# Kernel optimization log

Hardware: AMD Instinct MI355X
Metric: run time of the kernel (lower is better)

The kernel has to match this reference:

```python
import jax, jax.numpy as jnp
import numpy as np

NUM_NEIGHBORS = 1000

def setup_inputs() -> dict:
    key = jax.random.key(0)
    k1, k2, k3 = jax.random.split(key, 3)
    N, R, H, O = 1024, 100000, 512, 256
    x = jax.random.normal(k1, (N, H), dtype=jnp.float32)
    ref_x = jax.random.normal(k2, (R, H), dtype=jnp.float32)
    ref_y = jax.random.normal(k3, (R, O), dtype=jnp.float32)
    return {"x": x, "ref_x": ref_x, "ref_y": ref_y}

def reference(x, ref_x, ref_y):
    # encoder1 modeled as identity (x is the encoded embedding)
    xn = x / jnp.linalg.norm(x, axis=-1, keepdims=True)          # [N, H]
    rn = ref_x / jnp.linalg.norm(ref_x, axis=-1, keepdims=True)  # [R, H]
    sim = jnp.einsum('nh,rh->nr', xn, rn)                        # [N, R] cosine sims
    knn_vals, knn_idx = jax.lax.top_k(sim, NUM_NEIGHBORS)        # [N, K]
    weight = jax.nn.softmax(knn_vals, axis=1)                    # [N, K]
    neigh_y = ref_y[knn_idx]                                     # [N, K, O]
    pred_y = jnp.einsum('nko,nk->no', neigh_y, weight)           # [N, O]
    return pred_y
```

## Files before the change

kernel.cpp:

```cpp
#include <hip/hip_runtime.h>
#include <hip/hip_bf16.h>
#include <hip/hip_fp16.h>
#include <stdint.h>

#define NQ 1024
#define NR 100000
#define NH 512
#define NO 256
#define NK 1000
#define NBINS 4096
#define DEF_CAP 1024
#define CND_CAP 768
#define DELTA 2.0e-3f

typedef __attribute__((ext_vector_type(8))) short bf16x8;
typedef __attribute__((ext_vector_type(4))) float f32x4;
typedef __attribute__((address_space(3))) void lds_void;
typedef const __attribute__((address_space(1))) void glb_void;

static __device__ inline uint32_t pack_bf16_trunc(float lo, float hi) {
    return __builtin_amdgcn_perm(__float_as_uint(hi), __float_as_uint(lo), 0x07060302u);
}

__global__ __launch_bounds__(256) void conv_norm_kernel(const float* __restrict__ src,
                                                        int rows,
                                                        ushort* __restrict__ dst_bf,
                                                        double* __restrict__ inv_out)
{
    const int wave = threadIdx.x >> 6;
    const int lane = threadIdx.x & 63;
    const int row  = blockIdx.x * 4 + wave;
    if (row >= rows) return;
    const float* p = src + (size_t)row * NH + lane * 8;
    float4 v0 = *(const float4*)p;
    float4 v1 = *(const float4*)(p + 4);
    double s = (double)v0.x * v0.x + (double)v0.y * v0.y
             + (double)v0.z * v0.z + (double)v0.w * v0.w
             + (double)v1.x * v1.x + (double)v1.y * v1.y
             + (double)v1.z * v1.z + (double)v1.w * v1.w;
    uint4 pk;
    pk.x = pack_bf16_trunc(v0.x, v0.y);
    pk.y = pack_bf16_trunc(v0.z, v0.w);
    pk.z = pack_bf16_trunc(v1.x, v1.y);
    pk.w = pack_bf16_trunc(v1.z, v1.w);
    *(uint4*)(dst_bf + (size_t)row * NH + lane * 8) = pk;
    #pragma unroll
    for (int off = 32; off > 0; off >>= 1) s += __shfl_down(s, off, 64);
    if (lane == 0) inv_out[row] = 1.0 / sqrt(s);
}

__global__ __launch_bounds__(256) void conv_ry_kernel(const float* __restrict__ ry,
                                                      __half* __restrict__ ryh)
{
    const int wave = threadIdx.x >> 6;
    const int lane = threadIdx.x & 63;
    const int row  = blockIdx.x * 4 + wave;
    float4 v = *(const float4*)(ry + (size_t)row * NO + lane * 4);
    __half2 h01 = __floats2half2_rn(v.x, v.y);
    __half2 h23 = __floats2half2_rn(v.z, v.w);
    uint2 pk;
    pk.x = __builtin_bit_cast(uint32_t, h01);
    pk.y = __builtin_bit_cast(uint32_t, h23);
    *(uint2*)(ryh + (size_t)row * NO + lane * 4) = pk;
}

__global__ __launch_bounds__(256) void gemm_kernel(const ushort* __restrict__ xbf,
                                                   const ushort* __restrict__ rxbf,
                                                   const double* __restrict__ xinv,
                                                   const double* __restrict__ rinv,
                                                   __half* __restrict__ sim)
{
    __shared__ ushort a_lds[128 * 64];
    __shared__ ushort b_lds[128 * 64];
    const int bid = blockIdx.x;
    const int nt  = (bid & 7) + 8 * (bid >> 6);
    const int mt  = (bid >> 3) & 7;
    if (nt >= (NR + 127) / 128) return;
    const int m0 = mt * 128;
    const int r0 = nt * 128;

    const int tid  = threadIdx.x;
    const int lane = tid & 63;
    const int wave = tid >> 6;
    const int wq = (wave >> 1) * 64;
    const int wr = (wave & 1) * 64;

    f32x4 acc[4][4];
    #pragma unroll
    for (int i = 0; i < 4; ++i)
        #pragma unroll
        for (int j = 0; j < 4; ++j)
            #pragma unroll
            for (int r = 0; r < 4; ++r) acc[i][j][r] = 0.0f;

    const int srow  = lane >> 3;
    const int chunk = (lane & 7) ^ (srow & 7);

    for (int kt = 0; kt < NH; kt += 64) {
        #pragma unroll
        for (int ii = 0; ii < 4; ++ii) {
            const int inst = wave * 4 + ii;
            const int row  = inst * 8 + srow;
            const ushort* ga = xbf + (size_t)(m0 + row) * NH + kt + chunk * 8;
            __builtin_amdgcn_global_load_lds((glb_void*)ga,
                (lds_void*)(a_lds + inst * 512), 16, 0, 0);
            int rr = r0 + row; if (rr > NR - 1) rr = NR - 1;
            const ushort* gb = rxbf + (size_t)rr * NH + kt + chunk * 8;
            __builtin_amdgcn_global_load_lds((glb_void*)gb,
                (lds_void*)(b_lds + inst * 512), 16, 0, 0);
        }
        __syncthreads();
        #pragma unroll
        for (int kc = 0; kc < 2; ++kc) {
            const int c  = kc * 4 + (lane >> 4);
            const int px = (c ^ (lane & 7)) * 8;
            bf16x8 af[4], bfr[4];
            #pragma unroll
            for (int i = 0; i < 4; ++i)
                af[i] = *(const bf16x8*)&a_lds[(wq + i * 16 + (lane & 15)) * 64 + px];
            #pragma unroll
            for (int j = 0; j < 4; ++j)
                bfr[j] = *(const bf16x8*)&b_lds[(wr + j * 16 + (lane & 15)) * 64 + px];
            #pragma unroll
            for (int i = 0; i < 4; ++i)
                #pragma unroll
                for (int j = 0; j < 4; ++j)
                    acc[i][j] = __builtin_amdgcn_mfma_f32_16x16x32_bf16(af[i], bfr[j], acc[i][j], 0, 0, 0);
        }
        __syncthreads();
    }

    float xi[4][4];
    #pragma unroll
    for (int i = 0; i < 4; ++i) {
        int mb = m0 + wq + i * 16 + (lane >> 4) * 4;
        #pragma unroll
        for (int r = 0; r < 4; ++r) xi[i][r] = (float)xinv[mb + r];
    }
    #pragma unroll
    for (int j = 0; j < 4; ++j) {
        int nn = r0 + wr + j * 16 + (lane & 15);
        if (nn < NR) {
            float rv = (float)rinv[nn];
            #pragma unroll
            for (int i = 0; i < 4; ++i) {
                int mb = m0 + wq + i * 16 + (lane >> 4) * 4;
                #pragma unroll
                for (int r = 0; r < 4; ++r)
                    sim[(size_t)(mb + r) * NR + nn] = __float2half(acc[i][j][r] * xi[i][r] * rv);
            }
        }
    }
}

__global__ __launch_bounds__(256) void hist_collect_kernel(const __half* __restrict__ sim,
                                                           uint32_t* __restrict__ def_cnt,
                                                           uint32_t* __restrict__ cand_cnt,
                                                           float* __restrict__ def_val,
                                                           uint32_t* __restrict__ def_idx,
                                                           uint32_t* __restrict__ cand_idx)
{
    __shared__ uint32_t h[NBINS];
    __shared__ uint32_t ps[256];
    __shared__ float s_thi, s_tlo;
    __shared__ uint32_t s_dc, s_cc;
    const int n = blockIdx.x, tid = threadIdx.x;
    for (int b = tid; b < NBINS; b += 256) h[b] = 0u;
    __syncthreads();
    const uint4* row8 = (const uint4*)(sim + (size_t)n * NR);
    for (int i8 = tid; i8 < NR / 8; i8 += 256) {
        uint4 v = row8[i8];
        uint32_t ws[4] = {v.x, v.y, v.z, v.w};
        #pragma unroll
        for (int c = 0; c < 4; ++c) {
            float2 f = __half22float2(__builtin_bit_cast(__half2, ws[c]));
            int b0 = (int)((f.x + 1.0f) * 2048.0f); b0 = min(max(b0, 0), NBINS - 1); atomicAdd(&h[b0], 1u);
            int b1 = (int)((f.y + 1.0f) * 2048.0f); b1 = min(max(b1, 0), NBINS - 1); atomicAdd(&h[b1], 1u);
        }
    }
    __syncthreads();
    uint32_t cs = 0;
    #pragma unroll 4
    for (int b = 0; b < 16; ++b) cs += h[tid * 16 + b];
    ps[tid] = cs;
    __syncthreads();
    if (tid == 0) {
        uint32_t acc = 0; int tc = 0;
        for (int t2 = 255; t2 >= 0; --t2) {
            if (acc + ps[t2] >= (uint32_t)NK) { tc = t2; break; }
            acc += ps[t2];
        }
        int bstar = tc * 16;
        for (int b = tc * 16 + 15; b >= tc * 16; --b) {
            acc += h[b];
            if (acc >= (uint32_t)NK) { bstar = b; break; }
        }
        s_thi = (float)(bstar + 1) * (1.0f / 2048.0f) - 1.0f + DELTA;
        s_tlo = (float)bstar * (1.0f / 2048.0f) - 1.0f - DELTA;
        s_dc = 0u; s_cc = 0u;
    }
    __syncthreads();
    const float thi = s_thi, tlo = s_tlo;
    for (int i8 = tid; i8 < NR / 8; i8 += 256) {
        uint4 v = row8[i8];
        uint32_t ws[4] = {v.x, v.y, v.z, v.w};
        const int base = i8 * 8;
        #pragma unroll
        for (int c = 0; c < 4; ++c) {
            float2 f = __half22float2(__builtin_bit_cast(__half2, ws[c]));
            float sv[2] = {f.x, f.y};
            #pragma unroll
            for (int d = 0; d < 2; ++d) {
                float s = sv[d];
                if (s > thi) {
                    uint32_t p = atomicAdd(&s_dc, 1u);
                    if (p < DEF_CAP) {
                        def_val[(size_t)n * DEF_CAP + p] = s;
                        def_idx[(size_t)n * DEF_CAP + p] = (uint32_t)(base + c * 2 + d);
                    }
                } else if (s >= tlo) {
                    uint32_t p = atomicAdd(&s_cc, 1u);
                    if (p < CND_CAP) cand_idx[(size_t)n * CND_CAP + p] = (uint32_t)(base + c * 2 + d);
                }
            }
        }
    }
    __syncthreads();
    if (tid == 0) {
        def_cnt[n]  = s_dc < DEF_CAP ? s_dc : DEF_CAP;
        cand_cnt[n] = s_cc < CND_CAP ? s_cc : CND_CAP;
    }
}

__global__ __launch_bounds__(1024) void final_kernel(const float* __restrict__ x,
                                                     const float* __restrict__ rx,
                                                     const __half* __restrict__ ryh,
                                                     const double* __restrict__ xinv,
                                                     const double* __restrict__ rinv,
                                                     const uint32_t* __restrict__ def_cnt,
                                                     const uint32_t* __restrict__ cand_cnt,
                                                     const float* __restrict__ def_val,
                                                     const uint32_t* __restrict__ def_idx,
                                                     const uint32_t* __restrict__ cand_idx,
                                                     float* __restrict__ out)
{
    const int n = blockIdx.x, tid = threadIdx.x;
    const int lane = tid & 63, wave = tid >> 6;
    __shared__ double   cvd[CND_CAP];
    __shared__ uint32_t ci[CND_CAP];
    __shared__ float    sel_w[DEF_CAP];
    __shared__ uint32_t sel_idx[DEF_CAP];
    __shared__ float    red[1024];
    __shared__ float    s_r[16][256];
    __shared__ uint32_t s_sel;

    const int ca = (int)def_cnt[n];
    const int cb = (int)cand_cnt[n];
    int t = NK - ca; if (t > cb) t = cb; if (t < 0) t = 0;

    for (int j = tid; j < ca; j += 1024) {
        sel_w[j]   = def_val[(size_t)n * DEF_CAP + j];
        sel_idx[j] = def_idx[(size_t)n * DEF_CAP + j];
    }
    if (tid == 0) s_sel = 0u;

    const float* xr = x + (size_t)n * NH;
    for (int j = wave; j < cb; j += 16) {
        uint32_t idx = cand_idx[(size_t)n * CND_CAP + j];
        const float* rr = rx + (size_t)idx * NH;
        double s = 0.0;
        for (int h2 = lane; h2 < NH; h2 += 64)
            s += (double)xr[h2] * (double)rr[h2];
        #pragma unroll
        for (int off = 32; off > 0; off >>= 1) s += __shfl_down(s, off, 64);
        if (lane == 0) { cvd[j] = (s * xinv[n]) * rinv[idx]; ci[j] = idx; }
    }
    __syncthreads();

    if (tid < cb) {
        double vj = cvd[tid]; uint32_t ij = ci[tid];
        int rank = 0;
        for (int i = 0; i < cb; ++i) {
            double vi = cvd[i];
            rank += (vi > vj) || (vi == vj && ci[i] < ij);
        }
        if (rank < t) {
            uint32_t p = atomicAdd(&s_sel, 1u);
            sel_w[ca + p]   = (float)vj;
            sel_idx[ca + p] = ij;
        }
    }
    __syncthreads();
    const int M = ca + t;

    float lm = -3.0e38f;
    for (int k = tid; k < M; k += 1024) lm = fmaxf(lm, sel_w[k]);
    red[tid] = lm; __syncthreads();
    for (int off = 512; off > 0; off >>= 1) {
        if (tid < off) red[tid] = fmaxf(red[tid], red[tid + off]);
        __syncthreads();
    }
    const float mx = red[0];
    __syncthreads();
    float ls = 0.f;
    for (int k = tid; k < M; k += 1024) {
        float w = expf(sel_w[k] - mx);
        sel_w[k] = w;
        ls += w;
    }
    red[tid] = ls; __syncthreads();
    for (int off = 512; off > 0; off >>= 1) {
        if (tid < off) red[tid] += red[tid + off];
        __syncthreads();
    }
    const float wsum = red[0];
    __syncthreads();

    const int part = tid >> 6;
    float4 acc = make_float4(0.f, 0.f, 0.f, 0.f);
    for (int k = part; k < M; k += 16) {
        float w = sel_w[k];
        uint2 rv = *(const uint2*)(ryh + (size_t)sel_idx[k] * NO + lane * 4);
        float2 f01 = __half22float2(__builtin_bit_cast(__half2, rv.x));
        float2 f23 = __half22float2(__builtin_bit_cast(__half2, rv.y));
        acc.x = fmaf(w, f01.x, acc.x);
        acc.y = fmaf(w, f01.y, acc.y);
        acc.z = fmaf(w, f23.x, acc.z);
        acc.w = fmaf(w, f23.y, acc.w);
    }
    s_r[part][lane * 4 + 0] = acc.x;
    s_r[part][lane * 4 + 1] = acc.y;
    s_r[part][lane * 4 + 2] = acc.z;
    s_r[part][lane * 4 + 3] = acc.w;
    __syncthreads();
    if (tid < 256) {
        float s = 0.f;
        #pragma unroll
        for (int p = 0; p < 16; ++p) s += s_r[p][tid];
        out[(size_t)n * NO + tid] = s / wsum;
    }
}

extern "C" void kernel_launch(void* const* d_in, const int* in_sizes, int n_in,
                              void* d_out, int out_size, void* d_ws, size_t ws_size,
                              hipStream_t stream)
{
    const float* x  = (const float*)d_in[0];
    const float* rx = (const float*)d_in[1];
    const float* ry = (const float*)d_in[2];
    float* out = (float*)d_out;

    char* ws = (char*)d_ws;
    __half*   simh     = (__half*)(ws);
    ushort*   rxbf     = (ushort*)(ws + 204800000ull);
    __half*   ryh      = (__half*)(ws + 307200000ull);
    ushort*   xbf      = (ushort*)(ws + 358400000ull);
    double*   rinv     = (double*)(ws + 359448576ull);
    double*   xinv     = (double*)(ws + 360248576ull);
    uint32_t* def_cnt  = (uint32_t*)(ws + 360256768ull);
    uint32_t* cand_cnt = (uint32_t*)(ws + 360260864ull);
    float*    def_val  = (float*)(ws + 360264960ull);
    uint32_t* def_idx  = (uint32_t*)(ws + 364459264ull);
    uint32_t* cand_idx = (uint32_t*)(ws + 368653568ull);

    conv_norm_kernel<<<NQ / 4, 256, 0, stream>>>(x, NQ, xbf, xinv);
    conv_norm_kernel<<<NR / 4, 256, 0, stream>>>(rx, NR, rxbf, rinv);
    conv_ry_kernel<<<NR / 4, 256, 0, stream>>>(ry, ryh);
    gemm_kernel<<<6272, 256, 0, stream>>>(xbf, rxbf, xinv, rinv, simh);
    hist_collect_kernel<<<NQ, 256, 0, stream>>>(simh, def_cnt, cand_cnt,
                                                def_val, def_idx, cand_idx);
    final_kernel<<<NQ, 1024, 0, stream>>>(x, rx, ryh, xinv, rinv, def_cnt, cand_cnt,
                                          def_val, def_idx, cand_idx, out);
}
```

Before: 987.7 us.

## Replace per-row gather weighted sum with masked dense softmax-weight GEMM over all references

The final gather of the selected neighbors' ref_y rows is replaced by a dense fp16 MFMA GEMM. It multiplies masked exp(sim - max) weights over the full sim matrix by a transposed, padded ref_y, split along K and combined with atomic adds into an fp32 buffer. Candidates rejected by an exact-rank resolve pass are overwritten in sim with -2 so the threshold mask drops them. The softmax denominator is built from per-row sums taken during collection. This removes the scattered per-query gathers and the large def buffers, but adds a full read of the 200MB sim matrix, a ref_y transpose, and float atomics whose summation order is nondeterministic.

```diff
diff --git a/kernel.cpp b/kernel.cpp
--- a/kernel.cpp
+++ b/kernel.cpp
@@ -5,15 +5,16 @@
 
 #define NQ 1024
 #define NR 100000
+#define KPAD 100352
 #define NH 512
 #define NO 256
 #define NK 1000
 #define NBINS 4096
-#define DEF_CAP 1024
 #define CND_CAP 768
 #define DELTA 2.0e-3f
 
 typedef __attribute__((ext_vector_type(8))) short bf16x8;
+typedef __attribute__((ext_vector_type(8))) _Float16 f16x8;
 typedef __attribute__((ext_vector_type(4))) float f32x4;
 typedef __attribute__((address_space(3))) void lds_void;
 typedef const __attribute__((address_space(1))) void glb_void;
@@ -49,19 +50,32 @@
     if (lane == 0) inv_out[row] = 1.0 / sqrt(s);
 }
 
-__global__ __launch_bounds__(256) void conv_ry_kernel(const float* __restrict__ ry,
-                                                      __half* __restrict__ ryh)
-{
-    const int wave = threadIdx.x >> 6;
-    const int lane = threadIdx.x & 63;
-    const int row  = blockIdx.x * 4 + wave;
-    float4 v = *(const float4*)(ry + (size_t)row * NO + lane * 4);
-    __half2 h01 = __floats2half2_rn(v.x, v.y);
-    __half2 h23 = __floats2half2_rn(v.z, v.w);
-    uint2 pk;
-    pk.x = __builtin_bit_cast(uint32_t, h01);
-    pk.y = __builtin_bit_cast(uint32_t, h23);
-    *(uint2*)(ryh + (size_t)row * NO + lane * 4) = pk;
+__global__ __launch_bounds__(256) void conv_ryt_kernel(const float* __restrict__ ry,
+                                                       __half* __restrict__ ryT)
+{
+    __shared__ __half T[256][136];
+    const int r0 = blockIdx.x * 128;
+    #pragma unroll 4
+    for (int it = 0; it < 32; ++it) {
+        int slot = threadIdx.x + it * 256;
+        int row  = slot >> 6;
+        int c4   = (slot & 63) * 4;
+        int rr   = r0 + row;
+        float4 v = (rr < NR) ? *(const float4*)(ry + (size_t)rr * NO + c4)
+                             : make_float4(0.f, 0.f, 0.f, 0.f);
+        T[c4 + 0][row] = __float2half(v.x);
+        T[c4 + 1][row] = __float2half(v.y);
+        T[c4 + 2][row] = __float2half(v.z);
+        T[c4 + 3][row] = __float2half(v.w);
+    }
+    __syncthreads();
+    #pragma unroll 4
+    for (int it = 0; it < 16; ++it) {
+        int slot = threadIdx.x + it * 256;
+        int col  = slot >> 4;
+        int ch   = (slot & 15) * 8;
+        *(uint4*)(ryT + (size_t)col * KPAD + r0 + ch) = *(const uint4*)&T[col][ch];
+    }
 }
 
 __global__ __launch_bounds__(256) void gemm_kernel(const ushort* __restrict__ xbf,
@@ -155,25 +169,27 @@
 
 __global__ __launch_bounds__(256) void hist_collect_kernel(const __half* __restrict__ sim,
                                                            uint32_t* __restrict__ def_cnt,
+                                                           float* __restrict__ def_sum,
                                                            uint32_t* __restrict__ cand_cnt,
-                                                           float* __restrict__ def_val,
-                                                           uint32_t* __restrict__ def_idx,
-                                                           uint32_t* __restrict__ cand_idx)
+                                                           uint32_t* __restrict__ cand_idx,
+                                                           float* __restrict__ mx_out,
+                                                           float* __restrict__ tlo_out)
 {
     __shared__ uint32_t h[NBINS];
     __shared__ uint32_t ps[256];
-    __shared__ float s_thi, s_tlo;
-    __shared__ uint32_t s_dc, s_cc;
+    __shared__ float rf[256];
+    __shared__ float s_thi, s_tlo, s_mx;
+    __shared__ uint32_t s_cc;
     const int n = blockIdx.x, tid = threadIdx.x;
     for (int b = tid; b < NBINS; b += 256) h[b] = 0u;
     __syncthreads();
     const uint4* row8 = (const uint4*)(sim + (size_t)n * NR);
     for (int i8 = tid; i8 < NR / 8; i8 += 256) {
         uint4 v = row8[i8];
-        uint32_t ws[4] = {v.x, v.y, v.z, v.w};
+        uint32_t wv[4] = {v.x, v.y, v.z, v.w};
         #pragma unroll
         for (int c = 0; c < 4; ++c) {
-            float2 f = __half22float2(__builtin_bit_cast(__half2, ws[c]));
+            float2 f = __half22float2(__builtin_bit_cast(__half2, wv[c]));
             int b0 = (int)((f.x + 1.0f) * 2048.0f); b0 = min(max(b0, 0), NBINS - 1); atomicAdd(&h[b0], 1u);
             int b1 = (int)((f.y + 1.0f) * 2048.0f); b1 = min(max(b1, 0), NBINS - 1); atomicAdd(&h[b1], 1u);
         }
@@ -185,6 +201,11 @@
     ps[tid] = cs;
     __syncthreads();
     if (tid == 0) {
+        int gt = 255;
+        while (gt > 0 && ps[gt] == 0u) --gt;
+        int bt = gt * 16 + 15;
+        while (bt > gt * 16 && h[bt] == 0u) --bt;
+        s_mx = (float)(bt + 1) * (1.0f / 2048.0f) - 1.0f;
         uint32_t acc = 0; int tc = 0;
         for (int t2 = 255; t2 >= 0; --t2) {
             if (acc + ps[t2] >= (uint32_t)NK) { tc = t2; break; }
@@ -197,27 +218,26 @@
         }
         s_thi = (float)(bstar + 1) * (1.0f / 2048.0f) - 1.0f + DELTA;
         s_tlo = (float)bstar * (1.0f / 2048.0f) - 1.0f - DELTA;
-        s_dc = 0u; s_cc = 0u;
-    }
-    __syncthreads();
-    const float thi = s_thi, tlo = s_tlo;
+        s_cc = 0u;
+    }
+    __syncthreads();
+    const float thi = s_thi, tlo = s_tlo, mxv = s_mx;
+    float dsum = 0.f;
+    uint32_t dcnt = 0;
     for (int i8 = tid; i8 < NR / 8; i8 += 256) {
         uint4 v = row8[i8];
-        uint32_t ws[4] = {v.x, v.y, v.z, v.w};
+        uint32_t wv[4] = {v.x, v.y, v.z, v.w};
         const int base = i8 * 8;
         #pragma unroll
         for (int c = 0; c < 4; ++c) {
-            float2 f = __half22float2(__builtin_bit_cast(__half2, ws[c]));
+            float2 f = __half22float2(__builtin_bit_cast(__half2, wv[c]));
             float sv[2] = {f.x, f.y};
             #pragma unroll
             for (int d = 0; d < 2; ++d) {
                 float s = sv[d];
                 if (s > thi) {
-                    uint32_t p = atomicAdd(&s_dc, 1u);
-                    if (p < DEF_CAP) {
-                        def_val[(size_t)n * DEF_CAP + p] = s;
-                        def_idx[(size_t)n * DEF_CAP + p] = (uint32_t)(base + c * 2 + d);
-                    }
+                    dcnt++;
+                    dsum += __expf(s - mxv);
                 } else if (s >= tlo) {
                     uint32_t p = atomicAdd(&s_cc, 1u);
                     if (p < CND_CAP) cand_idx[(size_t)n * CND_CAP + p] = (uint32_t)(base + c * 2 + d);
@@ -225,47 +245,46 @@
             }
         }
     }
-    __syncthreads();
+    ps[tid] = dcnt; rf[tid] = dsum;
+    __syncthreads();
+    for (int off = 128; off > 0; off >>= 1) {
+        if (tid < off) { ps[tid] += ps[tid + off]; rf[tid] += rf[tid + off]; }
+        __syncthreads();
+    }
     if (tid == 0) {
-        def_cnt[n]  = s_dc < DEF_CAP ? s_dc : DEF_CAP;
+        def_cnt[n]  = ps[0];
+        def_sum[n]  = rf[0];
         cand_cnt[n] = s_cc < CND_CAP ? s_cc : CND_CAP;
-    }
-}
-
-__global__ __launch_bounds__(1024) void final_kernel(const float* __restrict__ x,
-                                                     const float* __restrict__ rx,
-                                                     const __half* __restrict__ ryh,
-                                                     const double* __restrict__ xinv,
-                                                     const double* __restrict__ rinv,
-                                                     const uint32_t* __restrict__ def_cnt,
-                                                     const uint32_t* __restrict__ cand_cnt,
-                                                     const float* __restrict__ def_val,
-                                                     const uint32_t* __restrict__ def_idx,
-                                                     const uint32_t* __restrict__ cand_idx,
-                                                     float* __restrict__ out)
+        mx_out[n]   = mxv;
+        tlo_out[n]  = tlo;
+    }
+}
+
+__global__ __launch_bounds__(256) void resolve_kernel(const float* __restrict__ x,
+                                                      const float* __restrict__ rx,
+                                                      const double* __restrict__ xinv,
+                                                      const double* __restrict__ rinv,
+                                                      const uint32_t* __restrict__ def_cnt,
+                                                      const float* __restrict__ def_sum,
+                                                      const uint32_t* __restrict__ cand_cnt,
+                                                      const uint32_t* __restrict__ cand_idx,
+                                                      const float* __restrict__ mx_in,
+                                                      __half* __restrict__ simh,
+                                                      float* __restrict__ wsum)
 {
     const int n = blockIdx.x, tid = threadIdx.x;
     const int lane = tid & 63, wave = tid >> 6;
     __shared__ double   cvd[CND_CAP];
     __shared__ uint32_t ci[CND_CAP];
-    __shared__ float    sel_w[DEF_CAP];
-    __shared__ uint32_t sel_idx[DEF_CAP];
-    __shared__ float    red[1024];
-    __shared__ float    s_r[16][256];
-    __shared__ uint32_t s_sel;
+    __shared__ float    red[256];
 
     const int ca = (int)def_cnt[n];
-    const int cb = (int)cand_cnt[n];
+    int cb = (int)cand_cnt[n]; if (cb > CND_CAP) cb = CND_CAP;
     int t = NK - ca; if (t > cb) t = cb; if (t < 0) t = 0;
-
-    for (int j = tid; j < ca; j += 1024) {
-        sel_w[j]   = def_val[(size_t)n * DEF_CAP + j];
-        sel_idx[j] = def_idx[(size_t)n * DEF_CAP + j];
-    }
-    if (tid == 0) s_sel = 0u;
+    const float mxv = mx_in[n];
 
     const float* xr = x + (size_t)n * NH;
-    for (int j = wave; j < cb; j += 16) {
+    for (int j = wave; j < cb; j += 4) {
         uint32_t idx = cand_idx[(size_t)n * CND_CAP + j];
         const float* rr = rx + (size_t)idx * NH;
         double s = 0.0;
@@ -277,68 +296,136 @@
     }
     __syncthreads();
 
-    if (tid < cb) {
-        double vj = cvd[tid]; uint32_t ij = ci[tid];
+    float wloc = 0.f;
+    for (int j = tid; j < cb; j += 256) {
+        double vj = cvd[j]; uint32_t ij = ci[j];
         int rank = 0;
         for (int i = 0; i < cb; ++i) {
             double vi = cvd[i];
             rank += (vi > vj) || (vi == vj && ci[i] < ij);
         }
+        float s = __half2float(simh[(size_t)n * NR + ij]);
         if (rank < t) {
-            uint32_t p = atomicAdd(&s_sel, 1u);
-            sel_w[ca + p]   = (float)vj;
-            sel_idx[ca + p] = ij;
-        }
-    }
-    __syncthreads();
-    const int M = ca + t;
-
-    float lm = -3.0e38f;
-    for (int k = tid; k < M; k += 1024) lm = fmaxf(lm, sel_w[k]);
-    red[tid] = lm; __syncthreads();
-    for (int off = 512; off > 0; off >>= 1) {
-        if (tid < off) red[tid] = fmaxf(red[tid], red[tid + off]);
-        __syncthreads();
-    }
-    const float mx = red[0];
-    __syncthreads();
-    float ls = 0.f;
-    for (int k = tid; k < M; k += 1024) {
-        float w = expf(sel_w[k] - mx);
-        sel_w[k] = w;
-        ls += w;
-    }
-    red[tid] = ls; __syncthreads();
-    for (int off = 512; off > 0; off >>= 1) {
+            wloc += __expf(s - mxv);
+        } else {
+            simh[(size_t)n * NR + ij] = __float2half(-2.0f);
+        }
+    }
+    red[tid] = wloc;
+    __syncthreads();
+    for (int off = 128; off > 0; off >>= 1) {
         if (tid < off) red[tid] += red[tid + off];
         __syncthreads();
     }
-    const float wsum = red[0];
-    __syncthreads();
-
-    const int part = tid >> 6;
-    float4 acc = make_float4(0.f, 0.f, 0.f, 0.f);
-    for (int k = part; k < M; k += 16) {
-        float w = sel_w[k];
-        uint2 rv = *(const uint2*)(ryh + (size_t)sel_idx[k] * NO + lane * 4);
-        float2 f01 = __half22float2(__builtin_bit_cast(__half2, rv.x));
-        float2 f23 = __half22float2(__builtin_bit_cast(__half2, rv.y));
-        acc.x = fmaf(w, f01.x, acc.x);
-        acc.y = fmaf(w, f01.y, acc.y);
-        acc.z = fmaf(w, f23.x, acc.z);
-        acc.w = fmaf(w, f23.y, acc.w);
-    }
-    s_r[part][lane * 4 + 0] = acc.x;
-    s_r[part][lane * 4 + 1] = acc.y;
-    s_r[part][lane * 4 + 2] = acc.z;
-    s_r[part][lane * 4 + 3] = acc.w;
-    __syncthreads();
-    if (tid < 256) {
-        float s = 0.f;
-        #pragma unroll
-        for (int p = 0; p < 16; ++p) s += s_r[p][tid];
-        out[(size_t)n * NO + tid] = s / wsum;
-    }
+    if (tid == 0) wsum[n] = def_sum[n] + red[0];
+}
+
+__global__ __launch_bounds__(256) void gemm2_kernel(const __half* __restrict__ simh,
+                                                    const __half* __restrict__ ryT,
+                                                    const float* __restrict__ tlo_in,
+                                                    const float* __restrict__ mx_in,
+                                                    float* __restrict__ accb)
+{
+    __shared__ _Float16 a_lds[128 * 64];
+    __shared__ _Float16 b_lds[128 * 64];
+    __shared__ float s_tlo[128], s_mx[128];
+
+    const int bid = blockIdx.x;
+    const int kt  = (bid & 7) + 8 * (bid >> 7);
+    const int mem = (bid >> 3) & 15;
+    const int mt  = mem & 7;
+    const int nt  = mem >> 3;
+    const int m0  = mt * 128;
+    const int n0  = nt * 128;
+    const int kb0 = kt * 3136;
+
+    const int tid  = threadIdx.x;
+    const int lane = tid & 63;
+    const int wave = tid >> 6;
+    const int wq = (wave >> 1) * 64;
+    const int wr = (wave & 1) * 64;
+    const int srow  = lane >> 3;
+    const int chunk = (lane & 7) ^ (srow & 7);
+
+    if (tid < 128) { s_tlo[tid] = tlo_in[m0 + tid]; s_mx[tid] = mx_in[m0 + tid]; }
+
+    f32x4 acc[4][4];
+    #pragma unroll
+    for (int i = 0; i < 4; ++i)
+        #pragma unroll
+        for (int j = 0; j < 4; ++j)
+            #pragma unroll
+            for (int r = 0; r < 4; ++r) acc[i][j][r] = 0.0f;
+    __syncthreads();
+
+    for (int ks = 0; ks < 49; ++ks) {
+        const int k0 = kb0 + ks * 64;
+        #pragma unroll
+        for (int ii = 0; ii < 4; ++ii) {
+            const int inst = wave * 4 + ii;
+            const int row  = inst * 8 + srow;
+            const __half* gb = ryT + (size_t)(n0 + row) * KPAD + k0 + chunk * 8;
+            __builtin_amdgcn_global_load_lds((glb_void*)gb,
+                (lds_void*)(b_lds + inst * 512), 16, 0, 0);
+        }
+        #pragma unroll
+        for (int i = 0; i < 4; ++i) {
+            int slot = tid + i * 256;
+            int row  = slot >> 3;
+            int c    = slot & 7;
+            int kg   = k0 + c * 8;
+            const __half* src = simh + (size_t)(m0 + row) * NR + (kg < NR ? kg : 0);
+            f16x8 sv = *(const f16x8*)src;
+            float tl = s_tlo[row], mv = s_mx[row];
+            f16x8 wv;
+            #pragma unroll
+            for (int j = 0; j < 8; ++j) {
+                float s = (float)sv[j];
+                float w = (kg + j < NR && s >= tl) ? __expf(s - mv) : 0.f;
+                wv[j] = (_Float16)w;
+            }
+            *(f16x8*)&a_lds[row * 64 + (c ^ (row & 7)) * 8] = wv;
+        }
+        __syncthreads();
+        #pragma unroll
+        for (int kc = 0; kc < 2; ++kc) {
+            const int c  = kc * 4 + (lane >> 4);
+            const int px = (c ^ (lane & 7)) * 8;
+            f16x8 af[4], bfr[4];
+            #pragma unroll
+            for (int i = 0; i < 4; ++i)
+                af[i] = *(const f16x8*)&a_lds[(wq + i * 16 + (lane & 15)) * 64 + px];
+            #pragma unroll
+            for (int j = 0; j < 4; ++j)
+                bfr[j] = *(const f16x8*)&b_lds[(wr + j * 16 + (lane & 15)) * 64 + px];
+            #pragma unroll
+            for (int i = 0; i < 4; ++i)
+                #pragma unroll
+                for (int j = 0; j < 4; ++j)
+                    acc[i][j] = __builtin_amdgcn_mfma_f32_16x16x32_f16(af[i], bfr[j], acc[i][j], 0, 0, 0);
+        }
+        __syncthreads();
+    }
+
+    #pragma unroll
+    for (int j = 0; j < 4; ++j) {
+        int nn = n0 + wr + j * 16 + (lane & 15);
+        #pragma unroll
+        for (int i = 0; i < 4; ++i) {
+            int mb = m0 + wq + i * 16 + (lane >> 4) * 4;
+            #pragma unroll
+            for (int r = 0; r < 4; ++r)
+                atomicAdd(&accb[(size_t)(mb + r) * NO + nn], acc[i][j][r]);
+        }
+    }
+}
+
+__global__ __launch_bounds__(256) void scale_kernel(const float* __restrict__ accb,
+                                                    const float* __restrict__ wsum,
+                                                    float* __restrict__ out)
+{
+    const int n = blockIdx.x;
+    out[(size_t)n * NO + threadIdx.x] = accb[(size_t)n * NO + threadIdx.x] / wsum[n];
 }
 
 extern "C" void kernel_launch(void* const* d_in, const int* in_sizes, int n_in,
@@ -353,22 +440,28 @@
     char* ws = (char*)d_ws;
     __half*   simh     = (__half*)(ws);
     ushort*   rxbf     = (ushort*)(ws + 204800000ull);
-    __half*   ryh      = (__half*)(ws + 307200000ull);
-    ushort*   xbf      = (ushort*)(ws + 358400000ull);
-    double*   rinv     = (double*)(ws + 359448576ull);
-    double*   xinv     = (double*)(ws + 360248576ull);
-    uint32_t* def_cnt  = (uint32_t*)(ws + 360256768ull);
-    uint32_t* cand_cnt = (uint32_t*)(ws + 360260864ull);
-    float*    def_val  = (float*)(ws + 360264960ull);
-    uint32_t* def_idx  = (uint32_t*)(ws + 364459264ull);
-    uint32_t* cand_idx = (uint32_t*)(ws + 368653568ull);
-
+    __half*   ryT      = (__half*)(ws + 307200000ull);
+    ushort*   xbf      = (ushort*)(ws + 358580224ull);
+    double*   rinv     = (double*)(ws + 359628800ull);
+    double*   xinv     = (double*)(ws + 360428800ull);
+    float*    mxv      = (float*)(ws + 360436992ull);
+    float*    tlov     = (float*)(ws + 360441088ull);
+    uint32_t* def_cnt  = (uint32_t*)(ws + 360445184ull);
+    float*    def_sum  = (float*)(ws + 360449280ull);
+    uint32_t* cand_cnt = (uint32_t*)(ws + 360453376ull);
+    float*    wsum     = (float*)(ws + 360457472ull);
+    float*    accb     = (float*)(ws + 360461568ull);
+    uint32_t* cand_idx = (uint32_t*)(ws + 361510144ull);
+
+    hipMemsetAsync(accb, 0, (size_t)NQ * NO * sizeof(float), stream);
     conv_norm_kernel<<<NQ / 4, 256, 0, stream>>>(x, NQ, xbf, xinv);
     conv_norm_kernel<<<NR / 4, 256, 0, stream>>>(rx, NR, rxbf, rinv);
-    conv_ry_kernel<<<NR / 4, 256, 0, stream>>>(ry, ryh);
+    conv_ryt_kernel<<<KPAD / 128, 256, 0, stream>>>(ry, ryT);
     gemm_kernel<<<6272, 256, 0, stream>>>(xbf, rxbf, xinv, rinv, simh);
-    hist_collect_kernel<<<NQ, 256, 0, stream>>>(simh, def_cnt, cand_cnt,
-                                                def_val, def_idx, cand_idx);
-    final_kernel<<<NQ, 1024, 0, stream>>>(x, rx, ryh, xinv, rinv, def_cnt, cand_cnt,
-                                          def_val, def_idx, cand_idx, out);
-}
+    hist_collect_kernel<<<NQ, 256, 0, stream>>>(simh, def_cnt, def_sum, cand_cnt,
+                                                cand_idx, mxv, tlov);
+    resolve_kernel<<<NQ, 256, 0, stream>>>(x, rx, xinv, rinv, def_cnt, def_sum,
+                                           cand_cnt, cand_idx, mxv, simh, wsum);
+    gemm2_kernel<<<512, 256, 0, stream>>>(simh, ryT, tlov, mxv, accb);
+    scale_kernel<<<NQ, 256, 0, stream>>>(accb, wsum, out);
+}
```

After: 1.213 ms. 22.8% more time.
